# Kernel optimization log

Measured on AMD Instinct MI355X. Metric: run time of the kernel, lower is better.

The kernel has to match this reference:

```python
import jax, jax.numpy as jnp
import numpy as np

B, S, HIDDEN = 1, 2048, 3584
NH, NKV, HD = 16, 8, 256
N_REP = NH // NKV
EPS = 1e-6
SCALING = 256.0 ** -0.5  # query_pre_attn_scalar=256
SOFTCAP = 50.0
NEG = -1e9


def rmsnorm(x, w):
    # Gemma RMSNorm with unit offset, computed in fp32
    xf = x.astype(jnp.float32)
    n = xf * jax.lax.rsqrt(jnp.mean(xf * xf, axis=-1, keepdims=True) + EPS)
    return (n * (1.0 + w.astype(jnp.float32))).astype(x.dtype)


def rope(x, cos, sin):
    # x: [B,S,H,D]; gemma pairs (x[:D/2], x[D/2:]) as complex (rotate-half)
    x1, x2 = jnp.split(x, 2, axis=-1)
    c = cos[None, :, None, :]
    s = sin[None, :, None, :]
    return jnp.concatenate([x1 * c - x2 * s, x1 * s + x2 * c], axis=-1).astype(x.dtype)


def setup_inputs() -> dict:
    key = jax.random.key(0)
    ks = jax.random.split(key, 6)
    hidden_states = jax.random.normal(ks[0], (B, S, HIDDEN), jnp.float32)
    w_qkv = jax.random.normal(ks[1], ((NH + 2 * NKV) * HD, HIDDEN), jnp.float32) * 0.02
    w_o = jax.random.normal(ks[2], (HIDDEN, NH * HD), jnp.float32) * 0.02
    q_norm_w = jax.random.normal(ks[3], (HD,), jnp.float32) * 0.1
    k_norm_w = jax.random.normal(ks[4], (HD,), jnp.float32) * 0.1
    k_cache = jnp.zeros((B, S, NKV, HD), jnp.float32)
    v_cache = jnp.zeros((B, S, NKV, HD), jnp.float32)
    kv_write_indices = jnp.arange(S, dtype=jnp.int32)
    # rotary tables, theta=10000
    inv_freq = 1.0 / (10000.0 ** (np.arange(0, HD, 2, dtype=np.float32) / HD))
    t = np.arange(S, dtype=np.float32)
    freqs = np.outer(t, inv_freq)  # [S, HD/2]
    cos = jnp.asarray(np.cos(freqs), jnp.float32)
    sin = jnp.asarray(np.sin(freqs), jnp.float32)
    # causal additive mask [1,1,S,S]
    causal = np.tril(np.ones((S, S), dtype=bool))
    mask = jnp.asarray(np.where(causal, 0.0, NEG).astype(np.float32))[None, None]
    return {"hidden_states": hidden_states, "cos": cos, "sin": sin,
            "kv_write_indices": kv_write_indices, "k_cache": k_cache,
            "v_cache": v_cache, "mask": mask, "w_qkv": w_qkv, "w_o": w_o,
            "q_norm_w": q_norm_w, "k_norm_w": k_norm_w}


def reference(hidden_states, cos, sin, kv_write_indices, k_cache, v_cache,
              mask, w_qkv, w_o, q_norm_w, k_norm_w):
    qkv = jnp.einsum('bsh,oh->bso', hidden_states, w_qkv)
    q_size, kv_size = NH * HD, NKV * HD
    xq = qkv[..., :q_size].reshape(B, S, NH, HD)
    xk = qkv[..., q_size:q_size + kv_size].reshape(B, S, NKV, HD)
    xv = qkv[..., q_size + kv_size:].reshape(B, S, NKV, HD)
    xq = rmsnorm(xq, q_norm_w)
    xk = rmsnorm(xk, k_norm_w)
    xq = rope(xq, cos, sin)
    xk = rope(xk, cos, sin)
    # KV cache write (index_copy_ along dim 1)
    kc = k_cache.at[:, kv_write_indices].set(xk)
    vc = v_cache.at[:, kv_write_indices].set(xv)
    # GQA expand
    key = jnp.repeat(kc, N_REP, axis=2)   # [B,S,NH,HD]
    val = jnp.repeat(vc, N_REP, axis=2)
    q = xq.transpose(0, 2, 1, 3) * SCALING  # [B,NH,S,HD]
    k = key.transpose(0, 2, 1, 3)
    v = val.transpose(0, 2, 1, 3)
    scores = jnp.einsum('bhqd,bhkd->bhqk', q, k)
    scores = jnp.tanh(scores / SOFTCAP) * SOFTCAP  # logit softcapping
    scores = scores + mask
    p = jax.nn.softmax(scores, axis=-1)
    out = jnp.einsum('bhqk,bhkd->bhqd', p, v)
    out = out.transpose(0, 2, 1, 3).reshape(B, S, NH * HD)
    return jnp.einsum('bsd,hd->bsh', out, w_o)
```

## Files before the change

### kernel.cpp

```cpp
#include <hip/hip_runtime.h>

typedef __bf16 bf16;
typedef __bf16 bf16x4 __attribute__((ext_vector_type(4)));
typedef __bf16 bf16x8 __attribute__((ext_vector_type(8)));
typedef float f32x4 __attribute__((ext_vector_type(4)));

#define S_LEN 2048
#define HID   3584
#define NHEADS 16
#define NKVH   8
#define HDIM   256
#define QKV_O  8192
#define O_IN   4096

typedef const __attribute__((address_space(1))) void* gp_t;
typedef __attribute__((address_space(3))) void* sp_t;

__device__ __forceinline__ void async16(const void* g, void* s) {
  __builtin_amdgcn_global_load_lds((gp_t)g, (sp_t)s, 16, 0, 0);
}

__device__ __forceinline__ f32x4 mfma16(bf16x8 a, bf16x8 b, f32x4 c) {
  return __builtin_amdgcn_mfma_f32_16x16x32_bf16(a, b, c, 0, 0, 0);
}

__global__ __launch_bounds__(256) void cast_kernel(const float* __restrict__ in,
                                                   bf16* __restrict__ out, int n4) {
  int i = blockIdx.x * 256 + threadIdx.x;
  if (i >= n4) return;
  f32x4 v = ((const f32x4*)in)[i];
  bf16x4 o = { (bf16)v[0], (bf16)v[1], (bf16)v[2], (bf16)v[3] };
  ((bf16x4*)out)[i] = o;
}

__global__ __launch_bounds__(256) void add2_kernel(const float* __restrict__ a,
                                                   const float* __restrict__ b,
                                                   float* __restrict__ o, int n4) {
  int i = blockIdx.x * 256 + threadIdx.x;
  if (i >= n4) return;
  f32x4 x = ((const f32x4*)a)[i];
  f32x4 y = ((const f32x4*)b)[i];
  ((f32x4*)o)[i] = x + y;
}

#define GSTG(gb, lb, kk, half, LDAB) do {                              \
    const bf16* _g = (gb) + (size_t)((half) * 128) * (LDAB) + (kk);    \
    bf16* _l = (lb) + (half) * 128 * 64 + soff;                        \
    async16(_g, _l);                                                   \
    async16(_g + (size_t)64 * (LDAB), _l + 64 * 64);                   \
  } while (0)
#define LD12(ab, bb, cx, ar, br) do {                                  \
    const bf16* _pa = (ab) + arow;                                     \
    const bf16* _pb = (bb) + brow;                                     \
    _Pragma("unroll")                                                  \
    for (int _i = 0; _i < 8; _i++) ar[_i] = *(const bf16x8*)(_pa + _i * 16 * 64 + (cx)); \
    _Pragma("unroll")                                                  \
    for (int _j = 0; _j < 4; _j++) br[_j] = *(const bf16x8*)(_pb + _j * 16 * 64 + (cx)); \
  } while (0)
#define MM32(ar, br) do {                                              \
    __builtin_amdgcn_s_setprio(1);                                     \
    _Pragma("unroll")                                                  \
    for (int _i = 0; _i < 8; _i++)                                     \
      _Pragma("unroll")                                                \
      for (int _j = 0; _j < 4; _j++)                                   \
        acc[_i][_j] = mfma16(ar[_i], br[_j], acc[_i][_j]);             \
    __builtin_amdgcn_s_setprio(0);                                     \
  } while (0)
#define BARS() do { __builtin_amdgcn_s_barrier(); __builtin_amdgcn_sched_barrier(0); } while (0)
#define LGKM0() asm volatile("s_waitcnt lgkmcnt(0)" ::: "memory")
#define WAITV8() asm volatile("s_waitcnt vmcnt(8)" ::: "memory")

#define GEMM_PIPE_BODY(LDAB)                                           \
  f32x4 acc[8][4];                                                     \
  _Pragma("unroll")                                                    \
  for (int i = 0; i < 8; i++)                                          \
    _Pragma("unroll")                                                  \
    for (int j = 0; j < 4; j++) { f32x4 z = {0.f, 0.f, 0.f, 0.f}; acc[i][j] = z; } \
  bf16x8 a0[8], b0[4], a1[8], b1[4];                                   \
  const int nT = K >> 6;                                               \
  const int nIter = K >> 7;                                            \
  GSTG(Ag, As0, 0, 0, LDAB); GSTG(Ag, As0, 0, 1, LDAB);                \
  GSTG(Bg, Bs0, 0, 0, LDAB); GSTG(Bg, Bs0, 0, 1, LDAB);                \
  GSTG(Ag, As1, 64, 0, LDAB); GSTG(Ag, As1, 64, 1, LDAB);              \
  GSTG(Bg, Bs1, 64, 0, LDAB); GSTG(Bg, Bs1, 64, 1, LDAB);              \
  WAITV8();                                                            \
  BARS();                                                              \
  LD12(As0, Bs0, c0, a0, b0);                                          \
  for (int t = 0; t < nIter; t++) {                                    \
    int t2 = 2 * t + 2; if (t2 > nT - 1) t2 = nT - 1;                  \
    int t3 = 2 * t + 3; if (t3 > nT - 1) t3 = nT - 1;                  \
    int k2 = t2 * 64, k3 = t3 * 64;                                    \
              \
    LD12(As0, Bs0, c1, a1, b1);                                        \
    MM32(a0, b0);                                                      \
    LGKM0();                                                           \
    BARS();                                                            \
                                \
    GSTG(Ag, As0, k2, 0, LDAB); GSTG(Ag, As0, k2, 1, LDAB);            \
    GSTG(Bg, Bs0, k2, 0, LDAB); GSTG(Bg, Bs0, k2, 1, LDAB);            \
    MM32(a1, b1);                                                      \
    WAITV8();                                                          \
    BARS();                                                            \
    LD12(As1, Bs1, c0, a0, b0);                                        \
                                             \
    LD12(As1, Bs1, c1, a1, b1);                                        \
    MM32(a0, b0);                                                      \
    LGKM0();                                                           \
    BARS();                                                            \
                                                              \
    GSTG(Ag, As1, k3, 0, LDAB); GSTG(Ag, As1, k3, 1, LDAB);            \
    GSTG(Bg, Bs1, k3, 0, LDAB); GSTG(Bg, Bs1, k3, 1, LDAB);            \
    MM32(a1, b1);                                                      \
    WAITV8();                                                          \
    BARS();                                                            \
    LD12(As0, Bs0, c0, a0, b0);                                        \
  }

__global__ __launch_bounds__(512, 2) void gemm_nt_8p(const bf16* __restrict__ A,
                                                     const bf16* __restrict__ B,
                                                     float* __restrict__ C,
                                                     int M, int N, int K) {
  __shared__ bf16 As0[256 * 64];
  __shared__ bf16 Bs0[256 * 64];
  __shared__ bf16 As1[256 * 64];
  __shared__ bf16 Bs1[256 * 64];
  int tid = threadIdx.x;
  int lane = tid & 63;
  int w = tid >> 6;
  int wm = w >> 2, wn = w & 3;
  int lid = blockIdx.x;
  int oid = (lid & 7) * 32 + (lid >> 3);
  int rect = oid >> 5, ri = oid & 31;
  int bm = (rect & 3) * 2 + (ri >> 4);
  int bn = (rect >> 2) * 16 + (ri & 15);
  int srow = tid >> 3, schunk = tid & 7;
  int gcol = (schunk ^ (srow & 7)) * 8;
  const bf16* Ag = A + (size_t)(bm * 256 + srow) * K + gcol;
  const bf16* Bg = B + (size_t)(bn * 256 + srow) * K + gcol;
  int soff = srow * 64 + schunk * 8;
  int fr = lane & 15, fq = lane >> 4;
  int c0 = ((fq) ^ (fr & 7)) * 8;
  int c1 = ((4 + fq) ^ (fr & 7)) * 8;
  const int arow = (wm * 128 + fr) * 64;
  const int brow = (wn * 64 + fr) * 64;

  GEMM_PIPE_BODY(K)

  int row0 = bm * 256 + wm * 128 + fq * 4;
  int col0 = bn * 256 + wn * 64 + fr;
#pragma unroll
  for (int i = 0; i < 8; i++)
#pragma unroll
    for (int j = 0; j < 4; j++)
#pragma unroll
      for (int r = 0; r < 4; r++)
        C[(size_t)(row0 + i * 16 + r) * N + col0 + j * 16] = acc[i][j][r];
}

__global__ __launch_bounds__(512, 2) void gemm_nt_8p_ks(const bf16* __restrict__ A,
                                                        const bf16* __restrict__ B,
                                                        float* __restrict__ C,
                                                        int M, int N, int K, int lda) {
  __shared__ bf16 As0[256 * 64];
  __shared__ bf16 Bs0[256 * 64];
  __shared__ bf16 As1[256 * 64];
  __shared__ bf16 Bs1[256 * 64];
  int tid = threadIdx.x;
  int lane = tid & 63;
  int w = tid >> 6;
  int wm = w >> 2, wn = w & 3;
  int lid = blockIdx.x;
  int ks = lid >= 112;
  int l2 = lid - ks * 112;
  int oid = (l2 & 7) * 14 + (l2 >> 3);
  int bm = oid / 14;
  int bn = oid - bm * 14;
  int kbase = ks * K;
  float* Cp = C + (size_t)ks * M * N;
  int srow = tid >> 3, schunk = tid & 7;
  int gcol = (schunk ^ (srow & 7)) * 8;
  const bf16* Ag = A + (size_t)(bm * 256 + srow) * lda + kbase + gcol;
  const bf16* Bg = B + (size_t)(bn * 256 + srow) * lda + kbase + gcol;
  int soff = srow * 64 + schunk * 8;
  int fr = lane & 15, fq = lane >> 4;
  int c0 = ((fq) ^ (fr & 7)) * 8;
  int c1 = ((4 + fq) ^ (fr & 7)) * 8;
  const int arow = (wm * 128 + fr) * 64;
  const int brow = (wn * 64 + fr) * 64;

  GEMM_PIPE_BODY(lda)

  int row0 = bm * 256 + wm * 128 + fq * 4;
  int col0 = bn * 256 + wn * 64 + fr;
#pragma unroll
  for (int i = 0; i < 8; i++)
#pragma unroll
    for (int j = 0; j < 4; j++)
#pragma unroll
      for (int r = 0; r < 4; r++)
        Cp[(size_t)(row0 + i * 16 + r) * N + col0 + j * 16] = acc[i][j][r];
}

__global__ __launch_bounds__(256) void qk_norm_rope(const float* __restrict__ qkv,
                                                    const float* __restrict__ cosb,
                                                    const float* __restrict__ sinb,
                                                    const float* __restrict__ qw,
                                                    const float* __restrict__ kw,
                                                    bf16* __restrict__ qout,
                                                    bf16* __restrict__ kout) {
  int s = blockIdx.x;
  int lane = threadIdx.x & 63;
  int w = threadIdx.x >> 6;
  int d0 = lane * 4;
  int dr = d0 & 127;
  f32x4 cv = *(const f32x4*)(cosb + s * 128 + dr);
  f32x4 sv = *(const f32x4*)(sinb + s * 128 + dr);
  bool hi = lane >= 32;
#pragma unroll
  for (int r = 0; r < 6; r++) {
    int head = r * 4 + w;
    const float* x = qkv + (size_t)s * QKV_O + head * HDIM + d0;
    f32x4 v = *(const f32x4*)x;
    float ss = v[0] * v[0] + v[1] * v[1] + v[2] * v[2] + v[3] * v[3];
#pragma unroll
    for (int off = 32; off > 0; off >>= 1) ss += __shfl_xor(ss, off);
    float scale = rsqrtf(ss * (1.0f / HDIM) + 1e-6f);
    bool isq = head < NHEADS;
    const float* wn = isq ? qw : kw;
    f32x4 wv = *(const f32x4*)(wn + d0);
    float y[4], o[4];
#pragma unroll
    for (int i = 0; i < 4; i++) y[i] = v[i] * scale * (1.0f + wv[i]);
#pragma unroll
    for (int i = 0; i < 4; i++) {
      float py = __shfl_xor(y[i], 32);
      o[i] = hi ? (py * sv[i] + y[i] * cv[i]) : (y[i] * cv[i] - py * sv[i]);
    }
    float mult = isq ? 0.0625f : 1.0f;
    bf16x4 ov = { (bf16)(o[0] * mult), (bf16)(o[1] * mult), (bf16)(o[2] * mult), (bf16)(o[3] * mult) };
    if (isq) *(bf16x4*)(qout + ((size_t)head * S_LEN + s) * HDIM + d0) = ov;
    else     *(bf16x4*)(kout + ((size_t)(head - NHEADS) * S_LEN + s) * HDIM + d0) = ov;
  }
}

__global__ __launch_bounds__(256) void v_transpose(const float* __restrict__ qkv, bf16* __restrict__ vt) {
  __shared__ float tile[64][65];
  int dt = blockIdx.x, st = blockIdx.y, h = blockIdx.z;
  int t = threadIdx.x;
  int d0 = dt * 64, s0 = st * 64;
#pragma unroll
  for (int i = 0; i < 16; i++) {
    int idx = i * 256 + t;
    int r = idx >> 6, c = idx & 63;
    tile[r][c] = qkv[(size_t)(s0 + r) * QKV_O + 6144 + h * HDIM + d0 + c];
  }
  __syncthreads();
#pragma unroll
  for (int i = 0; i < 16; i++) {
    int idx = i * 256 + t;
    int dr = idx >> 6, sc = idx & 63;
    vt[((size_t)h * HDIM + d0 + dr) * S_LEN + s0 + sc] = (bf16)tile[sc][dr];
  }
}

#define PSTRIDE 40
__global__ __launch_bounds__(256, 2) void attn_kernel(const bf16* __restrict__ q,
                                                      const bf16* __restrict__ kx,
                                                      const bf16* __restrict__ vt,
                                                      bf16* __restrict__ aout) {
  __shared__ bf16 kt[2][32 * 256];
  __shared__ bf16 vtile[2][256 * 32];
  __shared__ bf16 pbuf[4][16 * PSTRIDE];
  int h = blockIdx.x;
  int y = blockIdx.y;
  int qt = (y < 16) ? y : 47 - y;
  int kvh = h >> 1;
  int tid = threadIdx.x;
  int lane = tid & 63, w = tid >> 6;
  int fr = lane & 15, fq = lane >> 4;
  int qs = qt * 64;
  bf16x8 qf[8];
  const bf16* qb = q + ((size_t)h * S_LEN + qs + w * 16 + fr) * HDIM + fq * 8;
#pragma unroll
  for (int i = 0; i < 8; i++) qf[i] = *(const bf16x8*)(qb + i * 32);
  f32x4 acc[16];
#pragma unroll
  for (int i = 0; i < 16; i++) { f32x4 z = {0.f, 0.f, 0.f, 0.f}; acc[i] = z; }
  float lsum[4] = {0.f, 0.f, 0.f, 0.f};
  int krow = w * 2 + (lane >> 5);
  int kcolr = (lane & 31) * 8;
  const bf16* kg = kx + (size_t)kvh * S_LEN * HDIM;
  int vd = w * 16 + (lane >> 2);
  int vsw = (vd >> 1) & 3;
  int vcl = (lane & 3) * 8;
  int vcg = (((lane & 3) ^ vsw) * 8);
  const bf16* vg = vt + (size_t)kvh * HDIM * S_LEN;
  int rot0 = (fq * 8 - fr * 8) & 255;
  int rot1 = (fq * 8 - fr * 8 - 128) & 255;
  int fsw = (fr >> 1) & 3;
  int kmax = qs + 64;

#define ASTG(KK, B) do {                                                   \
    bf16* _kb = &kt[(B)][0]; bf16* _vb = &vtile[(B)][0];                   \
    _Pragma("unroll")                                                      \
    for (int p = 0; p < 4; p++) {                                          \
      int r = p * 8 + krow;                                                \
      int gc = (kcolr + r * 8) & 255;                                      \
      async16(kg + (size_t)((KK) + r) * HDIM + gc, _kb + r * 256 + kcolr); \
      int d = p * 64 + vd;                                                 \
      async16(vg + (size_t)d * S_LEN + (KK) + vcg, _vb + d * 32 + vcl);    \
    }                                                                      \
  } while (0)

  ASTG(0, 0);
  int ib = 0;
  for (int k0 = 0; k0 < kmax; k0 += 32, ib ^= 1) {
    __builtin_amdgcn_s_barrier();
    __builtin_amdgcn_sched_barrier(0);
    if (k0 + 32 < kmax) {
      ASTG(k0 + 32, ib ^ 1);
      asm volatile("s_waitcnt vmcnt(8)" ::: "memory");
    } else {
      asm volatile("s_waitcnt vmcnt(0)" ::: "memory");
    }
    __builtin_amdgcn_sched_barrier(0);
    __builtin_amdgcn_s_barrier();
    __builtin_amdgcn_sched_barrier(0);
    const bf16* ktb = &kt[ib][0];
    const bf16* vtb = &vtile[ib][0];
    const bf16* kt0 = ktb + fr * 256;
    const bf16* kt1 = ktb + (16 + fr) * 256;
    f32x4 s0 = {0.f, 0.f, 0.f, 0.f}, s1 = {0.f, 0.f, 0.f, 0.f};
    __builtin_amdgcn_s_setprio(1);
#pragma unroll
    for (int kk = 0; kk < 8; kk++) {
      bf16x8 b0 = *(const bf16x8*)(kt0 + ((kk * 32 + rot0) & 255));
      bf16x8 b1 = *(const bf16x8*)(kt1 + ((kk * 32 + rot1) & 255));
      s0 = mfma16(qf[kk], b0, s0);
      s1 = mfma16(qf[kk], b1, s1);
    }
    __builtin_amdgcn_s_setprio(0);
#pragma unroll
    for (int reg = 0; reg < 4; reg++) {
      int rowg = qs + w * 16 + fq * 4 + reg;
      float u0 = __builtin_amdgcn_exp2f(0.057707802f * s0[reg]);
      float u1 = __builtin_amdgcn_exp2f(0.057707802f * s1[reg]);
      float p0 = __builtin_amdgcn_exp2f(28.853901f - 144.26950f * __builtin_amdgcn_rcpf(u0 + 1.0f));
      float p1 = __builtin_amdgcn_exp2f(28.853901f - 144.26950f * __builtin_amdgcn_rcpf(u1 + 1.0f));
      p0 = (k0 + fr <= rowg) ? p0 : 0.0f;
      p1 = (k0 + 16 + fr <= rowg) ? p1 : 0.0f;
      lsum[reg] += p0 + p1;
      pbuf[w][(fq * 4 + reg) * PSTRIDE + fr] = (bf16)p0;
      pbuf[w][(fq * 4 + reg) * PSTRIDE + 16 + fr] = (bf16)p1;
    }
    bf16x8 pf = *(const bf16x8*)&pbuf[w][fr * PSTRIDE + fq * 8];
    __builtin_amdgcn_s_setprio(1);
#pragma unroll
    for (int ct = 0; ct < 16; ct++) {
      bf16x8 vf = *(const bf16x8*)&vtb[(ct * 16 + fr) * 32 + (fq ^ fsw) * 8];
      acc[ct] = mfma16(pf, vf, acc[ct]);
    }
    __builtin_amdgcn_s_setprio(0);
  }
#undef ASTG
  float rl[4];
#pragma unroll
  for (int reg = 0; reg < 4; reg++) {
    float l = lsum[reg];
    l += __shfl_xor(l, 1);
    l += __shfl_xor(l, 2);
    l += __shfl_xor(l, 4);
    l += __shfl_xor(l, 8);
    rl[reg] = 1.0f / l;
  }
#pragma unroll
  for (int ct = 0; ct < 16; ct++)
#pragma unroll
    for (int reg = 0; reg < 4; reg++)
      aout[(size_t)(qs + w * 16 + fq * 4 + reg) * O_IN + h * HDIM + ct * 16 + fr] =
          (bf16)(acc[ct][reg] * rl[reg]);
}

extern "C" void kernel_launch(void* const* d_in, const int* in_sizes, int n_in,
                              void* d_out, int out_size, void* d_ws, size_t ws_size,
                              hipStream_t stream) {
  const float* hidden = (const float*)d_in[0];
  const float* cosb   = (const float*)d_in[1];
  const float* sinb   = (const float*)d_in[2];
  const float* wqkv   = (const float*)d_in[7];
  const float* wo     = (const float*)d_in[8];
  const float* qnw    = (const float*)d_in[9];
  const float* knw    = (const float*)d_in[10];
  float* out = (float*)d_out;
  char* ws = (char*)d_ws;
  bf16*  h_bf    = (bf16*)(ws + 0);
  bf16*  wqkv_bf = (bf16*)(ws + 14680064);
  bf16*  wo_bf   = (bf16*)(ws + 73400320);
  float* qkv     = (float*)(ws + 102760448);
  bf16*  qb      = (bf16*)(ws + 169869312);
  bf16*  kb      = (bf16*)(ws + 186646528);
  bf16*  vtb     = (bf16*)(ws + 195035136);
  bf16*  attnb   = (bf16*)(ws + 203423744);
  float* part0   = (float*)(ws + 102760448);
  float* part1   = part0 + (size_t)2048 * 3584;

  cast_kernel<<<7168, 256, 0, stream>>>(hidden, h_bf, 1835008);
  cast_kernel<<<28672, 256, 0, stream>>>(wqkv, wqkv_bf, 7340032);
  cast_kernel<<<14336, 256, 0, stream>>>(wo, wo_bf, 3670016);
  gemm_nt_8p<<<256, 512, 0, stream>>>(h_bf, wqkv_bf, qkv, 2048, 8192, 3584);
  qk_norm_rope<<<2048, 256, 0, stream>>>(qkv, cosb, sinb, qnw, knw, qb, kb);
  v_transpose<<<dim3(4, 32, 8), 256, 0, stream>>>(qkv, vtb);
  attn_kernel<<<dim3(16, 32), 256, 0, stream>>>(qb, kb, vtb, attnb);
  gemm_nt_8p_ks<<<224, 512, 0, stream>>>(attnb, wo_bf, part0, 2048, 3584, 2048, 4096);
  add2_kernel<<<7168, 256, 0, stream>>>(part0, part1, out, 1835008);
}
```

Measured before the change: 580.0 us.

## Double query rows per attention block and merge cast launches into one kernel

```diff
diff --git a/kernel.cpp b/kernel.cpp
--- a/kernel.cpp
+++ b/kernel.cpp
@@ -24,23 +24,37 @@
   return __builtin_amdgcn_mfma_f32_16x16x32_bf16(a, b, c, 0, 0, 0);
 }
 
-__global__ __launch_bounds__(256) void cast_kernel(const float* __restrict__ in,
-                                                   bf16* __restrict__ out, int n4) {
-  int i = blockIdx.x * 256 + threadIdx.x;
-  if (i >= n4) return;
-  f32x4 v = ((const f32x4*)in)[i];
-  bf16x4 o = { (bf16)v[0], (bf16)v[1], (bf16)v[2], (bf16)v[3] };
-  ((bf16x4*)out)[i] = o;
+__global__ __launch_bounds__(256) void cast3_kernel(const float* __restrict__ a, bf16* __restrict__ oa, int na,
+                                                    const float* __restrict__ b, bf16* __restrict__ ob, int nb,
+                                                    const float* __restrict__ c, bf16* __restrict__ oc, int nc) {
+  int stride = gridDim.x * 256;
+  int t0 = blockIdx.x * 256 + threadIdx.x;
+  for (int i = t0; i < na; i += stride) {
+    f32x4 v = ((const f32x4*)a)[i];
+    bf16x4 o = { (bf16)v[0], (bf16)v[1], (bf16)v[2], (bf16)v[3] };
+    ((bf16x4*)oa)[i] = o;
+  }
+  for (int i = t0; i < nb; i += stride) {
+    f32x4 v = ((const f32x4*)b)[i];
+    bf16x4 o = { (bf16)v[0], (bf16)v[1], (bf16)v[2], (bf16)v[3] };
+    ((bf16x4*)ob)[i] = o;
+  }
+  for (int i = t0; i < nc; i += stride) {
+    f32x4 v = ((const f32x4*)c)[i];
+    bf16x4 o = { (bf16)v[0], (bf16)v[1], (bf16)v[2], (bf16)v[3] };
+    ((bf16x4*)oc)[i] = o;
+  }
 }
 
 __global__ __launch_bounds__(256) void add2_kernel(const float* __restrict__ a,
                                                    const float* __restrict__ b,
                                                    float* __restrict__ o, int n4) {
-  int i = blockIdx.x * 256 + threadIdx.x;
-  if (i >= n4) return;
-  f32x4 x = ((const f32x4*)a)[i];
-  f32x4 y = ((const f32x4*)b)[i];
-  ((f32x4*)o)[i] = x + y;
+  int stride = gridDim.x * 256;
+  for (int i = blockIdx.x * 256 + threadIdx.x; i < n4; i += stride) {
+    f32x4 x = ((const f32x4*)a)[i];
+    f32x4 y = ((const f32x4*)b)[i];
+    ((f32x4*)o)[i] = x + y;
+  }
 }
 
 #define GSTG(gb, lb, kk, half, LDAB) do {                              \
@@ -264,29 +278,30 @@
 }
 
 #define PSTRIDE 40
-__global__ __launch_bounds__(256, 2) void attn_kernel(const bf16* __restrict__ q,
-                                                      const bf16* __restrict__ kx,
-                                                      const bf16* __restrict__ vt,
-                                                      bf16* __restrict__ aout) {
+__global__ __launch_bounds__(256) void attn_kernel(const bf16* __restrict__ q,
+                                                   const bf16* __restrict__ kx,
+                                                   const bf16* __restrict__ vt,
+                                                   bf16* __restrict__ aout) {
   __shared__ bf16 kt[2][32 * 256];
   __shared__ bf16 vtile[2][256 * 32];
-  __shared__ bf16 pbuf[4][16 * PSTRIDE];
+  __shared__ bf16 pbuf[4][2][16 * PSTRIDE];
   int h = blockIdx.x;
-  int y = blockIdx.y;
-  int qt = (y < 16) ? y : 47 - y;
+  int qt = blockIdx.y;
   int kvh = h >> 1;
   int tid = threadIdx.x;
   int lane = tid & 63, w = tid >> 6;
   int fr = lane & 15, fq = lane >> 4;
-  int qs = qt * 64;
-  bf16x8 qf[8];
-  const bf16* qb = q + ((size_t)h * S_LEN + qs + w * 16 + fr) * HDIM + fq * 8;
-#pragma unroll
-  for (int i = 0; i < 8; i++) qf[i] = *(const bf16x8*)(qb + i * 32);
-  f32x4 acc[16];
-#pragma unroll
-  for (int i = 0; i < 16; i++) { f32x4 z = {0.f, 0.f, 0.f, 0.f}; acc[i] = z; }
-  float lsum[4] = {0.f, 0.f, 0.f, 0.f};
+  int qs = qt * 128;
+  bf16x8 qfA[8], qfB[8];
+  const bf16* qbA = q + ((size_t)h * S_LEN + qs + w * 32 + fr) * HDIM + fq * 8;
+  const bf16* qbB = qbA + (size_t)16 * HDIM;
+#pragma unroll
+  for (int i = 0; i < 8; i++) { qfA[i] = *(const bf16x8*)(qbA + i * 32); qfB[i] = *(const bf16x8*)(qbB + i * 32); }
+  f32x4 accA[16], accB[16];
+#pragma unroll
+  for (int i = 0; i < 16; i++) { f32x4 z = {0.f, 0.f, 0.f, 0.f}; accA[i] = z; accB[i] = z; }
+  float lsumA[4] = {0.f, 0.f, 0.f, 0.f};
+  float lsumB[4] = {0.f, 0.f, 0.f, 0.f};
   int krow = w * 2 + (lane >> 5);
   int kcolr = (lane & 31) * 8;
   const bf16* kg = kx + (size_t)kvh * S_LEN * HDIM;
@@ -298,7 +313,7 @@
   int rot0 = (fq * 8 - fr * 8) & 255;
   int rot1 = (fq * 8 - fr * 8 - 128) & 255;
   int fsw = (fr >> 1) & 3;
-  int kmax = qs + 64;
+  int kmax = qs + 128;
 
 #define ASTG(KK, B) do {                                                   \
     bf16* _kb = &kt[(B)][0]; bf16* _vb = &vtile[(B)][0];                   \
@@ -330,55 +345,78 @@
     const bf16* vtb = &vtile[ib][0];
     const bf16* kt0 = ktb + fr * 256;
     const bf16* kt1 = ktb + (16 + fr) * 256;
-    f32x4 s0 = {0.f, 0.f, 0.f, 0.f}, s1 = {0.f, 0.f, 0.f, 0.f};
+    f32x4 s0a = {0.f, 0.f, 0.f, 0.f}, s1a = {0.f, 0.f, 0.f, 0.f};
+    f32x4 s0b = {0.f, 0.f, 0.f, 0.f}, s1b = {0.f, 0.f, 0.f, 0.f};
     __builtin_amdgcn_s_setprio(1);
 #pragma unroll
     for (int kk = 0; kk < 8; kk++) {
       bf16x8 b0 = *(const bf16x8*)(kt0 + ((kk * 32 + rot0) & 255));
       bf16x8 b1 = *(const bf16x8*)(kt1 + ((kk * 32 + rot1) & 255));
-      s0 = mfma16(qf[kk], b0, s0);
-      s1 = mfma16(qf[kk], b1, s1);
+      s0a = mfma16(qfA[kk], b0, s0a);
+      s1a = mfma16(qfA[kk], b1, s1a);
+      s0b = mfma16(qfB[kk], b0, s0b);
+      s1b = mfma16(qfB[kk], b1, s1b);
     }
     __builtin_amdgcn_s_setprio(0);
 #pragma unroll
     for (int reg = 0; reg < 4; reg++) {
-      int rowg = qs + w * 16 + fq * 4 + reg;
-      float u0 = __builtin_amdgcn_exp2f(0.057707802f * s0[reg]);
-      float u1 = __builtin_amdgcn_exp2f(0.057707802f * s1[reg]);
+      int rowgA = qs + w * 32 + fq * 4 + reg;
+      int rowgB = rowgA + 16;
+      float u0 = __builtin_amdgcn_exp2f(0.057707802f * s0a[reg]);
+      float u1 = __builtin_amdgcn_exp2f(0.057707802f * s1a[reg]);
       float p0 = __builtin_amdgcn_exp2f(28.853901f - 144.26950f * __builtin_amdgcn_rcpf(u0 + 1.0f));
       float p1 = __builtin_amdgcn_exp2f(28.853901f - 144.26950f * __builtin_amdgcn_rcpf(u1 + 1.0f));
-      p0 = (k0 + fr <= rowg) ? p0 : 0.0f;
-      p1 = (k0 + 16 + fr <= rowg) ? p1 : 0.0f;
-      lsum[reg] += p0 + p1;
-      pbuf[w][(fq * 4 + reg) * PSTRIDE + fr] = (bf16)p0;
-      pbuf[w][(fq * 4 + reg) * PSTRIDE + 16 + fr] = (bf16)p1;
-    }
-    bf16x8 pf = *(const bf16x8*)&pbuf[w][fr * PSTRIDE + fq * 8];
+      p0 = (k0 + fr <= rowgA) ? p0 : 0.0f;
+      p1 = (k0 + 16 + fr <= rowgA) ? p1 : 0.0f;
+      lsumA[reg] += p0 + p1;
+      pbuf[w][0][(fq * 4 + reg) * PSTRIDE + fr] = (bf16)p0;
+      pbuf[w][0][(fq * 4 + reg) * PSTRIDE + 16 + fr] = (bf16)p1;
+      float v0 = __builtin_amdgcn_exp2f(0.057707802f * s0b[reg]);
+      float v1 = __builtin_amdgcn_exp2f(0.057707802f * s1b[reg]);
+      float q0 = __builtin_amdgcn_exp2f(28.853901f - 144.26950f * __builtin_amdgcn_rcpf(v0 + 1.0f));
+      float q1 = __builtin_amdgcn_exp2f(28.853901f - 144.26950f * __builtin_amdgcn_rcpf(v1 + 1.0f));
+      q0 = (k0 + fr <= rowgB) ? q0 : 0.0f;
+      q1 = (k0 + 16 + fr <= rowgB) ? q1 : 0.0f;
+      lsumB[reg] += q0 + q1;
+      pbuf[w][1][(fq * 4 + reg) * PSTRIDE + fr] = (bf16)q0;
+      pbuf[w][1][(fq * 4 + reg) * PSTRIDE + 16 + fr] = (bf16)q1;
+    }
+    bf16x8 pfA = *(const bf16x8*)&pbuf[w][0][fr * PSTRIDE + fq * 8];
+    bf16x8 pfB = *(const bf16x8*)&pbuf[w][1][fr * PSTRIDE + fq * 8];
     __builtin_amdgcn_s_setprio(1);
 #pragma unroll
     for (int ct = 0; ct < 16; ct++) {
       bf16x8 vf = *(const bf16x8*)&vtb[(ct * 16 + fr) * 32 + (fq ^ fsw) * 8];
-      acc[ct] = mfma16(pf, vf, acc[ct]);
+      accA[ct] = mfma16(pfA, vf, accA[ct]);
+      accB[ct] = mfma16(pfB, vf, accB[ct]);
     }
     __builtin_amdgcn_s_setprio(0);
   }
 #undef ASTG
-  float rl[4];
+  float rlA[4], rlB[4];
 #pragma unroll
   for (int reg = 0; reg < 4; reg++) {
-    float l = lsum[reg];
-    l += __shfl_xor(l, 1);
-    l += __shfl_xor(l, 2);
-    l += __shfl_xor(l, 4);
-    l += __shfl_xor(l, 8);
-    rl[reg] = 1.0f / l;
+    float la = lsumA[reg];
+    la += __shfl_xor(la, 1);
+    la += __shfl_xor(la, 2);
+    la += __shfl_xor(la, 4);
+    la += __shfl_xor(la, 8);
+    rlA[reg] = 1.0f / la;
+    float lb = lsumB[reg];
+    lb += __shfl_xor(lb, 1);
+    lb += __shfl_xor(lb, 2);
+    lb += __shfl_xor(lb, 4);
+    lb += __shfl_xor(lb, 8);
+    rlB[reg] = 1.0f / lb;
   }
 #pragma unroll
   for (int ct = 0; ct < 16; ct++)
 #pragma unroll
-    for (int reg = 0; reg < 4; reg++)
-      aout[(size_t)(qs + w * 16 + fq * 4 + reg) * O_IN + h * HDIM + ct * 16 + fr] =
-          (bf16)(acc[ct][reg] * rl[reg]);
+    for (int reg = 0; reg < 4; reg++) {
+      int rowA = qs + w * 32 + fq * 4 + reg;
+      aout[(size_t)rowA * O_IN + h * HDIM + ct * 16 + fr] = (bf16)(accA[ct][reg] * rlA[reg]);
+      aout[(size_t)(rowA + 16) * O_IN + h * HDIM + ct * 16 + fr] = (bf16)(accB[ct][reg] * rlB[reg]);
+    }
 }
 
 extern "C" void kernel_launch(void* const* d_in, const int* in_sizes, int n_in,
@@ -404,13 +442,13 @@
   float* part0   = (float*)(ws + 102760448);
   float* part1   = part0 + (size_t)2048 * 3584;
 
-  cast_kernel<<<7168, 256, 0, stream>>>(hidden, h_bf, 1835008);
-  cast_kernel<<<28672, 256, 0, stream>>>(wqkv, wqkv_bf, 7340032);
-  cast_kernel<<<14336, 256, 0, stream>>>(wo, wo_bf, 3670016);
+  cast3_kernel<<<2048, 256, 0, stream>>>(hidden, h_bf, 1835008,
+                                         wqkv, wqkv_bf, 7340032,
+                                         wo, wo_bf, 3670016);
   gemm_nt_8p<<<256, 512, 0, stream>>>(h_bf, wqkv_bf, qkv, 2048, 8192, 3584);
   qk_norm_rope<<<2048, 256, 0, stream>>>(qkv, cosb, sinb, qnw, knw, qb, kb);
   v_transpose<<<dim3(4, 32, 8), 256, 0, stream>>>(qkv, vtb);
-  attn_kernel<<<dim3(16, 32), 256, 0, stream>>>(qb, kb, vtb, attnb);
+  attn_kernel<<<dim3(16, 16), 256, 0, stream>>>(qb, kb, vtb, attnb);
   gemm_nt_8p_ks<<<224, 512, 0, stream>>>(attnb, wo_bf, part0, 2048, 3584, 2048, 4096);
-  add2_kernel<<<7168, 256, 0, stream>>>(part0, part1, out, 1835008);
-}
+  add2_kernel<<<2048, 256, 0, stream>>>(part0, part1, out, 1835008);
+}
```

New measurement: 630.8 us. 8.7% more time.

## Split attention tile across 8 waves and merge cast launches

Applied to the files above, without the earlier changes.

```diff
diff --git a/kernel.cpp b/kernel.cpp
--- a/kernel.cpp
+++ b/kernel.cpp
@@ -24,23 +24,37 @@
   return __builtin_amdgcn_mfma_f32_16x16x32_bf16(a, b, c, 0, 0, 0);
 }
 
-__global__ __launch_bounds__(256) void cast_kernel(const float* __restrict__ in,
-                                                   bf16* __restrict__ out, int n4) {
-  int i = blockIdx.x * 256 + threadIdx.x;
-  if (i >= n4) return;
-  f32x4 v = ((const f32x4*)in)[i];
-  bf16x4 o = { (bf16)v[0], (bf16)v[1], (bf16)v[2], (bf16)v[3] };
-  ((bf16x4*)out)[i] = o;
+__global__ __launch_bounds__(256) void cast3_kernel(const float* __restrict__ a, bf16* __restrict__ oa, int na,
+                                                    const float* __restrict__ b, bf16* __restrict__ ob, int nb,
+                                                    const float* __restrict__ c, bf16* __restrict__ oc, int nc) {
+  int stride = gridDim.x * 256;
+  int t0 = blockIdx.x * 256 + threadIdx.x;
+  for (int i = t0; i < na; i += stride) {
+    f32x4 v = ((const f32x4*)a)[i];
+    bf16x4 o = { (bf16)v[0], (bf16)v[1], (bf16)v[2], (bf16)v[3] };
+    ((bf16x4*)oa)[i] = o;
+  }
+  for (int i = t0; i < nb; i += stride) {
+    f32x4 v = ((const f32x4*)b)[i];
+    bf16x4 o = { (bf16)v[0], (bf16)v[1], (bf16)v[2], (bf16)v[3] };
+    ((bf16x4*)ob)[i] = o;
+  }
+  for (int i = t0; i < nc; i += stride) {
+    f32x4 v = ((const f32x4*)c)[i];
+    bf16x4 o = { (bf16)v[0], (bf16)v[1], (bf16)v[2], (bf16)v[3] };
+    ((bf16x4*)oc)[i] = o;
+  }
 }
 
 __global__ __launch_bounds__(256) void add2_kernel(const float* __restrict__ a,
                                                    const float* __restrict__ b,
                                                    float* __restrict__ o, int n4) {
-  int i = blockIdx.x * 256 + threadIdx.x;
-  if (i >= n4) return;
-  f32x4 x = ((const f32x4*)a)[i];
-  f32x4 y = ((const f32x4*)b)[i];
-  ((f32x4*)o)[i] = x + y;
+  int stride = gridDim.x * 256;
+  for (int i = blockIdx.x * 256 + threadIdx.x; i < n4; i += stride) {
+    f32x4 x = ((const f32x4*)a)[i];
+    f32x4 y = ((const f32x4*)b)[i];
+    ((f32x4*)o)[i] = x + y;
+  }
 }
 
 #define GSTG(gb, lb, kk, half, LDAB) do {                              \
@@ -90,24 +104,20 @@
     int t2 = 2 * t + 2; if (t2 > nT - 1) t2 = nT - 1;                  \
     int t3 = 2 * t + 3; if (t3 > nT - 1) t3 = nT - 1;                  \
     int k2 = t2 * 64, k3 = t3 * 64;                                    \
-              \
     LD12(As0, Bs0, c1, a1, b1);                                        \
     MM32(a0, b0);                                                      \
     LGKM0();                                                           \
     BARS();                                                            \
-                                \
     GSTG(Ag, As0, k2, 0, LDAB); GSTG(Ag, As0, k2, 1, LDAB);            \
     GSTG(Bg, Bs0, k2, 0, LDAB); GSTG(Bg, Bs0, k2, 1, LDAB);            \
     MM32(a1, b1);                                                      \
     WAITV8();                                                          \
     BARS();                                                            \
     LD12(As1, Bs1, c0, a0, b0);                                        \
-                                             \
     LD12(As1, Bs1, c1, a1, b1);                                        \
     MM32(a0, b0);                                                      \
     LGKM0();                                                           \
     BARS();                                                            \
-                                                              \
     GSTG(Ag, As1, k3, 0, LDAB); GSTG(Ag, As1, k3, 1, LDAB);            \
     GSTG(Bg, Bs1, k3, 0, LDAB); GSTG(Bg, Bs1, k3, 1, LDAB);            \
     MM32(a1, b1);                                                      \
@@ -264,28 +274,31 @@
 }
 
 #define PSTRIDE 40
-__global__ __launch_bounds__(256, 2) void attn_kernel(const bf16* __restrict__ q,
+__global__ __launch_bounds__(512, 4) void attn_kernel(const bf16* __restrict__ q,
                                                       const bf16* __restrict__ kx,
                                                       const bf16* __restrict__ vt,
                                                       bf16* __restrict__ aout) {
   __shared__ bf16 kt[2][32 * 256];
   __shared__ bf16 vtile[2][256 * 32];
   __shared__ bf16 pbuf[4][16 * PSTRIDE];
+  __shared__ float lred[8][16];
   int h = blockIdx.x;
   int y = blockIdx.y;
   int qt = (y < 16) ? y : 47 - y;
   int kvh = h >> 1;
   int tid = threadIdx.x;
   int lane = tid & 63, w = tid >> 6;
+  int wr = w & 3;
+  int gB = w >> 2;
   int fr = lane & 15, fq = lane >> 4;
   int qs = qt * 64;
   bf16x8 qf[8];
-  const bf16* qb = q + ((size_t)h * S_LEN + qs + w * 16 + fr) * HDIM + fq * 8;
+  const bf16* qb = q + ((size_t)h * S_LEN + qs + wr * 16 + fr) * HDIM + fq * 8;
 #pragma unroll
   for (int i = 0; i < 8; i++) qf[i] = *(const bf16x8*)(qb + i * 32);
-  f32x4 acc[16];
-#pragma unroll
-  for (int i = 0; i < 16; i++) { f32x4 z = {0.f, 0.f, 0.f, 0.f}; acc[i] = z; }
+  f32x4 acc[8];
+#pragma unroll
+  for (int i = 0; i < 8; i++) { f32x4 z = {0.f, 0.f, 0.f, 0.f}; acc[i] = z; }
   float lsum[4] = {0.f, 0.f, 0.f, 0.f};
   int krow = w * 2 + (lane >> 5);
   int kcolr = (lane & 31) * 8;
@@ -295,19 +308,19 @@
   int vcl = (lane & 3) * 8;
   int vcg = (((lane & 3) ^ vsw) * 8);
   const bf16* vg = vt + (size_t)kvh * HDIM * S_LEN;
-  int rot0 = (fq * 8 - fr * 8) & 255;
-  int rot1 = (fq * 8 - fr * 8 - 128) & 255;
+  int rot = gB ? ((fq * 8 - fr * 8 - 128) & 255) : ((fq * 8 - fr * 8) & 255);
+  int ktrow = gB * 16 + fr;
   int fsw = (fr >> 1) & 3;
   int kmax = qs + 64;
 
 #define ASTG(KK, B) do {                                                   \
     bf16* _kb = &kt[(B)][0]; bf16* _vb = &vtile[(B)][0];                   \
     _Pragma("unroll")                                                      \
-    for (int p = 0; p < 4; p++) {                                          \
-      int r = p * 8 + krow;                                                \
+    for (int p = 0; p < 2; p++) {                                          \
+      int r = p * 16 + krow;                                               \
       int gc = (kcolr + r * 8) & 255;                                      \
       async16(kg + (size_t)((KK) + r) * HDIM + gc, _kb + r * 256 + kcolr); \
-      int d = p * 64 + vd;                                                 \
+      int d = p * 128 + vd;                                                \
       async16(vg + (size_t)d * S_LEN + (KK) + vcg, _vb + d * 32 + vcl);    \
     }                                                                      \
   } while (0)
@@ -319,7 +332,7 @@
     __builtin_amdgcn_sched_barrier(0);
     if (k0 + 32 < kmax) {
       ASTG(k0 + 32, ib ^ 1);
-      asm volatile("s_waitcnt vmcnt(8)" ::: "memory");
+      asm volatile("s_waitcnt vmcnt(4)" ::: "memory");
     } else {
       asm volatile("s_waitcnt vmcnt(0)" ::: "memory");
     }
@@ -328,42 +341,40 @@
     __builtin_amdgcn_sched_barrier(0);
     const bf16* ktb = &kt[ib][0];
     const bf16* vtb = &vtile[ib][0];
-    const bf16* kt0 = ktb + fr * 256;
-    const bf16* kt1 = ktb + (16 + fr) * 256;
-    f32x4 s0 = {0.f, 0.f, 0.f, 0.f}, s1 = {0.f, 0.f, 0.f, 0.f};
+    const bf16* ktg = ktb + ktrow * 256;
+    f32x4 s = {0.f, 0.f, 0.f, 0.f};
     __builtin_amdgcn_s_setprio(1);
 #pragma unroll
     for (int kk = 0; kk < 8; kk++) {
-      bf16x8 b0 = *(const bf16x8*)(kt0 + ((kk * 32 + rot0) & 255));
-      bf16x8 b1 = *(const bf16x8*)(kt1 + ((kk * 32 + rot1) & 255));
-      s0 = mfma16(qf[kk], b0, s0);
-      s1 = mfma16(qf[kk], b1, s1);
+      bf16x8 b0 = *(const bf16x8*)(ktg + ((kk * 32 + rot) & 255));
+      s = mfma16(qf[kk], b0, s);
     }
     __builtin_amdgcn_s_setprio(0);
+    int cbase = k0 + gB * 16;
 #pragma unroll
     for (int reg = 0; reg < 4; reg++) {
-      int rowg = qs + w * 16 + fq * 4 + reg;
-      float u0 = __builtin_amdgcn_exp2f(0.057707802f * s0[reg]);
-      float u1 = __builtin_amdgcn_exp2f(0.057707802f * s1[reg]);
-      float p0 = __builtin_amdgcn_exp2f(28.853901f - 144.26950f * __builtin_amdgcn_rcpf(u0 + 1.0f));
-      float p1 = __builtin_amdgcn_exp2f(28.853901f - 144.26950f * __builtin_amdgcn_rcpf(u1 + 1.0f));
-      p0 = (k0 + fr <= rowg) ? p0 : 0.0f;
-      p1 = (k0 + 16 + fr <= rowg) ? p1 : 0.0f;
-      lsum[reg] += p0 + p1;
-      pbuf[w][(fq * 4 + reg) * PSTRIDE + fr] = (bf16)p0;
-      pbuf[w][(fq * 4 + reg) * PSTRIDE + 16 + fr] = (bf16)p1;
+      int rowg = qs + wr * 16 + fq * 4 + reg;
+      float u = __builtin_amdgcn_exp2f(0.057707802f * s[reg]);
+      float p = __builtin_amdgcn_exp2f(28.853901f - 144.26950f * __builtin_amdgcn_rcpf(u + 1.0f));
+      p = (cbase + fr <= rowg) ? p : 0.0f;
+      lsum[reg] += p;
+      pbuf[wr][(fq * 4 + reg) * PSTRIDE + gB * 16 + fr] = (bf16)p;
     }
-    bf16x8 pf = *(const bf16x8*)&pbuf[w][fr * PSTRIDE + fq * 8];
+    asm volatile("s_waitcnt lgkmcnt(0)" ::: "memory");
+    __builtin_amdgcn_s_barrier();
+    __builtin_amdgcn_sched_barrier(0);
+    bf16x8 pf = *(const bf16x8*)&pbuf[wr][fr * PSTRIDE + fq * 8];
     __builtin_amdgcn_s_setprio(1);
 #pragma unroll
-    for (int ct = 0; ct < 16; ct++) {
-      bf16x8 vf = *(const bf16x8*)&vtb[(ct * 16 + fr) * 32 + (fq ^ fsw) * 8];
+    for (int ct = 0; ct < 8; ct++) {
+      int cte = gB * 8 + ct;
+      bf16x8 vf = *(const bf16x8*)&vtb[(cte * 16 + fr) * 32 + (fq ^ fsw) * 8];
       acc[ct] = mfma16(pf, vf, acc[ct]);
     }
     __builtin_amdgcn_s_setprio(0);
   }
 #undef ASTG
-  float rl[4];
+  float lown[4];
 #pragma unroll
   for (int reg = 0; reg < 4; reg++) {
     float l = lsum[reg];
@@ -371,14 +382,24 @@
     l += __shfl_xor(l, 2);
     l += __shfl_xor(l, 4);
     l += __shfl_xor(l, 8);
-    rl[reg] = 1.0f / l;
-  }
-#pragma unroll
-  for (int ct = 0; ct < 16; ct++)
+    lown[reg] = l;
+    if (fr == 0) lred[w][fq * 4 + reg] = l;
+  }
+  asm volatile("s_waitcnt lgkmcnt(0)" ::: "memory");
+  __builtin_amdgcn_s_barrier();
+  __builtin_amdgcn_sched_barrier(0);
+  float rl[4];
+#pragma unroll
+  for (int reg = 0; reg < 4; reg++)
+    rl[reg] = 1.0f / (lown[reg] + lred[w ^ 4][fq * 4 + reg]);
+#pragma unroll
+  for (int ct = 0; ct < 8; ct++) {
+    int cte = gB * 8 + ct;
 #pragma unroll
     for (int reg = 0; reg < 4; reg++)
-      aout[(size_t)(qs + w * 16 + fq * 4 + reg) * O_IN + h * HDIM + ct * 16 + fr] =
+      aout[(size_t)(qs + wr * 16 + fq * 4 + reg) * O_IN + h * HDIM + cte * 16 + fr] =
           (bf16)(acc[ct][reg] * rl[reg]);
+  }
 }
 
 extern "C" void kernel_launch(void* const* d_in, const int* in_sizes, int n_in,
@@ -404,13 +425,13 @@
   float* part0   = (float*)(ws + 102760448);
   float* part1   = part0 + (size_t)2048 * 3584;
 
-  cast_kernel<<<7168, 256, 0, stream>>>(hidden, h_bf, 1835008);
-  cast_kernel<<<28672, 256, 0, stream>>>(wqkv, wqkv_bf, 7340032);
-  cast_kernel<<<14336, 256, 0, stream>>>(wo, wo_bf, 3670016);
+  cast3_kernel<<<2048, 256, 0, stream>>>(hidden, h_bf, 1835008,
+                                         wqkv, wqkv_bf, 7340032,
+                                         wo, wo_bf, 3670016);
   gemm_nt_8p<<<256, 512, 0, stream>>>(h_bf, wqkv_bf, qkv, 2048, 8192, 3584);
   qk_norm_rope<<<2048, 256, 0, stream>>>(qkv, cosb, sinb, qnw, knw, qb, kb);
   v_transpose<<<dim3(4, 32, 8), 256, 0, stream>>>(qkv, vtb);
-  attn_kernel<<<dim3(16, 32), 256, 0, stream>>>(qb, kb, vtb, attnb);
+  attn_kernel<<<dim3(16, 32), 512, 0, stream>>>(qb, kb, vtb, attnb);
   gemm_nt_8p_ks<<<224, 512, 0, stream>>>(attnb, wo_bf, part0, 2048, 3584, 2048, 4096);
-  add2_kernel<<<7168, 256, 0, stream>>>(part0, part1, out, 1835008);
-}
+  add2_kernel<<<2048, 256, 0, stream>>>(part0, part1, out, 1835008);
+}
```

Result: no change. 574.0 us (-1.0%).
